# Kernel optimization log

Hardware: AMD Instinct MI355X
Metric: run time of the kernel (lower is better)

The kernel has to match this reference:

```python
import jax, jax.numpy as jnp
import numpy as np

# ---- constants mirroring ATSSPostProcessor defaults / metainfo ----
PRE_NMS_THRESH = 0.05
PRE_NMS_TOP_N = 1000
NMS_THRESH = 0.6
POST_TOP_N = 100
IMG_H, IMG_W = 800.0, 1216.0      # metainfo img_shape
BW_XY, BW_WH = 10.0, 5.0          # GLIP/ATSS box coder weights (10,10,5,5)
MAX_DWH = float(np.log(1000.0 / 16.0))
CLASS_OFFSET = 10000.0            # batched_nms class offset (> max coord)


def setup_inputs() -> dict:
    key = jax.random.key(0)
    k0, k1, k2, k3 = jax.random.split(key, 4)
    N, C, L, H, W = 8, 80, 256, 100, 152
    box_regression = jax.random.normal(k0, (N, 4, H, W), jnp.float32)
    centerness = jax.random.normal(k1, (N, 1, H, W), jnp.float32)
    box_cls = jax.random.normal(k2, (N, C, H, W), jnp.float32)
    dot_product_logits = jax.random.normal(k3, (N, H * W, L), jnp.float32)
    # stride-8 grid anchors with base size 64
    ys, xs = np.meshgrid(np.arange(H), np.arange(W), indexing='ij')
    cx, cy = (xs + 0.5) * 8.0, (ys + 0.5) * 8.0
    anchors = jnp.asarray(
        np.stack([cx - 32, cy - 32, cx + 32, cy + 32], -1).reshape(-1, 4),
        jnp.float32)
    # MEAN aggregation positive map: class j <- tokens [3j, 3j+1, 3j+2]
    pm = np.zeros((C, L), np.float32)
    for j in range(C):
        pm[j, 3 * j:3 * j + 3] = 1.0 / 3.0
    pos_map = jnp.asarray(pm)
    return dict(box_regression=box_regression, centerness=centerness,
                box_cls=box_cls, dot_product_logits=dot_product_logits,
                anchors=anchors, pos_map=pos_map)


def _decode(a, r):
    # delta_xywh decode with weights (10,10,5,5), clamped to img_shape
    aw, ah = a[..., 2] - a[..., 0], a[..., 3] - a[..., 1]
    acx, acy = a[..., 0] + 0.5 * aw, a[..., 1] + 0.5 * ah
    dx, dy = r[..., 0] / BW_XY, r[..., 1] / BW_XY
    dw = jnp.minimum(r[..., 2] / BW_WH, MAX_DWH)
    dh = jnp.minimum(r[..., 3] / BW_WH, MAX_DWH)
    pcx, pcy = dx * aw + acx, dy * ah + acy
    pw, ph = jnp.exp(dw) * aw, jnp.exp(dh) * ah
    x1 = jnp.clip(pcx - 0.5 * pw, 0.0, IMG_W)
    y1 = jnp.clip(pcy - 0.5 * ph, 0.0, IMG_H)
    x2 = jnp.clip(pcx + 0.5 * pw, 0.0, IMG_W)
    y2 = jnp.clip(pcy + 0.5 * ph, 0.0, IMG_H)
    return jnp.stack([x1, y1, x2, y2], -1)


def _iou_matrix(b):  # b: [K,4]
    area = (b[:, 2] - b[:, 0]) * (b[:, 3] - b[:, 1])
    ix1 = jnp.maximum(b[:, None, 0], b[None, :, 0])
    iy1 = jnp.maximum(b[:, None, 1], b[None, :, 1])
    ix2 = jnp.minimum(b[:, None, 2], b[None, :, 2])
    iy2 = jnp.minimum(b[:, None, 3], b[None, :, 3])
    inter = jnp.maximum(ix2 - ix1, 0.0) * jnp.maximum(iy2 - iy1, 0.0)
    return inter / (area[:, None] + area[None, :] - inter + 1e-6)


def _nms_single(boxes, scores, labels, valid):
    # class-aware greedy NMS (batched_nms) on fixed-size K candidates
    K = boxes.shape[0]
    s = jnp.where(valid, scores, -1.0)
    order = jnp.argsort(-s)
    b, s, l, v = boxes[order], s[order], labels[order], valid[order]
    ob = b + (l.astype(b.dtype) * CLASS_OFFSET)[:, None]
    iou = _iou_matrix(ob)
    ar = jnp.arange(K)

    def body(i, keep):
        sup = keep[i] & (iou[i] > NMS_THRESH) & (ar > i)
        return keep & ~sup

    keep = jax.lax.fori_loop(0, K, body, v)
    s2 = jnp.where(keep, s, -1.0)
    topv, topi = jax.lax.top_k(s2, POST_TOP_N)
    good = topv > 0.0
    fb = jnp.where(good[:, None], b[topi], 0.0)
    fs = jnp.where(good, topv, 0.0)
    fl = jnp.where(good, l[topi], 0)
    return fb, fs, fl


def reference(box_regression, centerness, box_cls, dot_product_logits,
              anchors, pos_map):
    N = box_regression.shape[0]
    C = pos_map.shape[0]
    HW = anchors.shape[0]
    # permute_and_flatten: [N,4,H,W] -> [N,HW,4]
    reg = box_regression.transpose(0, 2, 3, 1).reshape(N, HW, 4)
    ctr = jax.nn.sigmoid(centerness.reshape(N, HW))
    # sigmoid score fusion + MEAN grounding->od aggregation
    dp = jax.nn.sigmoid(dot_product_logits)            # [N,HW,L]
    scores = jnp.einsum('nkl,cl->nkc', dp, pos_map)    # [N,HW,C]
    cand = scores > PRE_NMS_THRESH
    fused = scores * ctr[:, :, None]
    # dynamic per-image topk over candidates == fixed-K masked top_k
    masked = jnp.where(cand, fused, -1.0).reshape(N, HW * C)
    vals, idx = jax.lax.top_k(masked, PRE_NMS_TOP_N)   # [N,K]
    valid = jnp.take_along_axis(cand.reshape(N, -1), idx, axis=1)
    loc = idx // C
    labels = idx % C + 1
    a = anchors[loc]                                           # [N,K,4]
    r = jnp.take_along_axis(reg, loc[..., None], axis=1)       # [N,K,4]
    boxes = _decode(a, r)
    sc = jnp.sqrt(jnp.maximum(vals, 0.0))
    w = boxes[..., 2] - boxes[..., 0]
    h = boxes[..., 3] - boxes[..., 1]
    valid = valid & (w > 0) & (h > 0)  # min_size = 0 filter
    # scale_factor = 1.0 -> boxes unchanged
    out_boxes, out_scores, out_labels = jax.vmap(_nms_single)(
        boxes, sc, labels, valid)
    return out_boxes, out_scores, out_labels
```

## Files before the change

kernel.cpp:

```cpp
#include <hip/hip_runtime.h>
#include <hip/hip_bf16.h>

#define NIMG 8
#define NC   80
#define NL   256
#define HWQ  15200
#define TOPK 1000
#define CAP  4096
#define SSORT 2048
#define NPOST 100
#define PERIMG (HWQ * NC)
#define TOTAL (NIMG * PERIMG)
#define SROW 32
#define SBLK32 (NIMG * HWQ / SROW)
#define PI4  (PERIMG / 4)
#define WPI  (PI4 / 64)
#define NWAVE (NIMG * WPI)
#define CBLK (TOTAL / 4 / 256)

__device__ __forceinline__ unsigned flipKey(float f) {
    unsigned u = __float_as_uint(f);
    return u ^ (((unsigned)((int)u >> 31)) | 0x80000000u);
}
__device__ __forceinline__ float unflipKey(unsigned k) {
    unsigned u = k ^ ((k & 0x80000000u) ? 0x80000000u : 0xFFFFFFFFu);
    return __uint_as_float(u);
}
__device__ __forceinline__ float sigmoidf(float x) {
    return 1.0f / (1.0f + expf(-x));
}

__global__ void __launch_bounds__(256)
kinit(const float* __restrict__ pm, unsigned* nnz, unsigned* tok, float* wt,
      unsigned* __restrict__ gh) {
    int g = blockIdx.x * 256 + threadIdx.x;
    if (g < NIMG * 4096) gh[g] = 0;
    if (g < NC) {
        int c = g;
        int cnt = 0;
        for (int l = 0; l < NL; ++l) {
            float v = pm[c * NL + l];
            if (v != 0.0f) { tok[cnt * NC + c] = l; wt[cnt * NC + c] = v; cnt++; }
        }
        nnz[c] = cnt;
    }
}

__global__ void __launch_bounds__(512)
kscoreh(const float* __restrict__ dp, const float* __restrict__ cent,
        const unsigned* __restrict__ nnz, const unsigned* __restrict__ tok,
        const float* __restrict__ wt, float* __restrict__ scores,
        unsigned* __restrict__ gh) {
    __shared__ unsigned h[4096];
    __shared__ float sctr[SROW];
    int t = threadIdx.x;
    for (int i = t; i < 4096; i += 512) h[i] = 0;
    long long base = (long long)blockIdx.x * SROW;
    if (t < SROW) sctr[t] = sigmoidf(cent[base + t]);
    long long obase = base * NC;
    const float* dpb = dp + base * NL;

    int  rr[5], cc[5], mm[5];
    int  tk[5][3];
    float wv[5][3], xv[5][3];
#pragma unroll
    for (int j = 0; j < 5; ++j) {
        int o = t + j * 512;
        rr[j] = o / NC; cc[j] = o - rr[j] * NC;
        mm[j] = (int)nnz[cc[j]];
        int c = cc[j];
        tk[j][0] = (int)tok[c] & 255;
        tk[j][1] = (int)tok[NC + c] & 255;
        tk[j][2] = (int)tok[2 * NC + c] & 255;
        wv[j][0] = wt[c]; wv[j][1] = wt[NC + c]; wv[j][2] = wt[2 * NC + c];
    }
#pragma unroll
    for (int j = 0; j < 5; ++j) {
        const float* row = dpb + rr[j] * NL;
        if (tk[j][1] == tk[j][0] + 1 && tk[j][2] == tk[j][0] + 2) {
            float3 v3 = *(const float3*)(row + tk[j][0]);
            xv[j][0] = v3.x; xv[j][1] = v3.y; xv[j][2] = v3.z;
        } else {
            xv[j][0] = row[tk[j][0]];
            xv[j][1] = row[tk[j][1]];
            xv[j][2] = row[tk[j][2]];
        }
    }
    __syncthreads();
#pragma unroll
    for (int j = 0; j < 5; ++j) {
        float acc = 0.0f;
        if (mm[j] == 3) {
            float s0 = sigmoidf(xv[j][0]);
            float s1 = sigmoidf(xv[j][1]);
            float s2 = sigmoidf(xv[j][2]);
            acc += s0 * wv[j][0]; acc += s1 * wv[j][1]; acc += s2 * wv[j][2];
        } else {
            const float* row = dpb + rr[j] * NL;
            for (int q = 0; q < mm[j]; ++q)
                acc += sigmoidf(row[tok[q * NC + cc[j]]]) * wt[q * NC + cc[j]];
        }
        float sc = (acc > 0.05f) ? acc * sctr[rr[j]] : -1.0f;
        scores[obase + t + j * 512] = sc;
        atomicAdd(&h[flipKey(sc) >> 20], 1u);
    }
    __syncthreads();
    int n = (int)(base / HWQ);
    for (int i = t; i < 4096; i += 512)
        if (h[i]) atomicAdd(&gh[n * 4096 + i], h[i]);
}

__global__ void kfind1(const unsigned* __restrict__ gh, unsigned* meta) {
    __shared__ unsigned h[4096];
    __shared__ unsigned psum[256];
    int n = blockIdx.x;
    for (int i = threadIdx.x; i < 4096; i += 256) h[i] = gh[n * 4096 + i];
    __syncthreads();
    unsigned s = 0;
    for (int i = 0; i < 16; ++i) s += h[threadIdx.x * 16 + i];
    psum[threadIdx.x] = s;
    __syncthreads();
    if (threadIdx.x == 0) {
        unsigned cum = 0, above = 0; int B = 0; bool done = false;
        for (int seg = 255; seg >= 0 && !done; --seg) {
            if (cum + psum[seg] >= TOPK) {
                for (int b = seg * 16 + 15; b >= seg * 16; --b) {
                    if (cum + h[b] >= TOPK) { B = b; above = cum; done = true; break; }
                    cum += h[b];
                }
            } else cum += psum[seg];
        }
        meta[n] = (unsigned)B;
        meta[8 + n] = above;
    }
}

__global__ void __launch_bounds__(256)
kcountM(const float4* __restrict__ scores4, const unsigned* __restrict__ meta,
        unsigned* __restrict__ wavecnt, unsigned long long* __restrict__ wavemask) {
    int i4 = blockIdx.x * 256 + threadIdx.x;
    int n = i4 / PI4;
    unsigned B = meta[n];
    float4 v = scores4[i4];
    bool s0 = (flipKey(v.x) >> 20) >= B;
    bool s1 = (flipKey(v.y) >> 20) >= B;
    bool s2 = (flipKey(v.z) >> 20) >= B;
    bool s3 = (flipKey(v.w) >> 20) >= B;
    unsigned long long m0 = __ballot(s0);
    unsigned long long m1 = __ballot(s1);
    unsigned long long m2 = __ballot(s2);
    unsigned long long m3 = __ballot(s3);
    if ((threadIdx.x & 63) == 0) {
        int w = i4 >> 6;
        wavemask[(size_t)w * 4 + 0] = m0;
        wavemask[(size_t)w * 4 + 1] = m1;
        wavemask[(size_t)w * 4 + 2] = m2;
        wavemask[(size_t)w * 4 + 3] = m3;
        wavecnt[w] = (unsigned)(__popcll(m0) + __popcll(m1)
                              + __popcll(m2) + __popcll(m3));
    }
}

__global__ void __launch_bounds__(1024)
kgather(const unsigned* __restrict__ wavecnt,
        const unsigned long long* __restrict__ wavemask,
        const float* __restrict__ scores, const unsigned* __restrict__ meta,
        unsigned long long* __restrict__ cand,
        unsigned long long* __restrict__ sorted) {
    __shared__ unsigned ps16[17];
    __shared__ unsigned long long sbuf[SSORT];
    __shared__ unsigned h[4096];
    __shared__ unsigned psum[256];
    __shared__ unsigned selcnt, Fbin;
    int n = blockIdx.x, t = threadIdx.x;
    int lane = t & 63, wid = t >> 6;
    const unsigned* wc = wavecnt + n * WPI;
    const unsigned long long* wm = wavemask + (size_t)n * WPI * 4;
    const float* sb = scores + (size_t)n * PERIMG;
    sbuf[t] = 0ULL; sbuf[t + 1024] = 0ULL;

    int s0 = t * 5;
    unsigned loc[5], vv[5]; unsigned sum = 0;
#pragma unroll
    for (int j = 0; j < 5; ++j) {
        int i = s0 + j;
        unsigned x = (i < WPI) ? wc[i] : 0u;
        vv[j] = x; loc[j] = sum; sum += x;
    }
    unsigned wincl = sum;
#pragma unroll
    for (int off = 1; off < 64; off <<= 1) {
        unsigned o = (unsigned)__shfl_up((int)wincl, off);
        if (lane >= off) wincl += o;
    }
    if (lane == 63) ps16[wid] = wincl;
    __syncthreads();
    if (t == 0) {
        unsigned c = 0;
        for (int w = 0; w < 16; ++w) { unsigned x = ps16[w]; ps16[w] = c; c += x; }
        ps16[16] = c;
    }
    __syncthreads();
    unsigned excl = ps16[wid] + (wincl - sum);
    unsigned total = ps16[16];
    int nsel;

    if (total <= SSORT) {
#pragma unroll
        for (int j = 0; j < 5; ++j) {
            int wl = s0 + j;
            if (wl < WPI && vv[j]) {
                unsigned off = excl + loc[j];
                const unsigned long long* mk = wm + (size_t)wl * 4;
#pragma unroll
                for (int e = 0; e < 4; ++e) {
                    unsigned long long m = mk[e];
                    while (m) {
                        int b = __ffsll(m) - 1; m &= m - 1;
                        int li = wl * 256 + b * 4 + e;
                        unsigned key = flipKey(sb[li]);
                        sbuf[off++] = ((unsigned long long)key << 32)
                                      | (unsigned)(~li);
                    }
                }
            }
        }
        nsel = (int)total;
        __syncthreads();
    } else {
        unsigned long long* cb = cand + (size_t)n * CAP;
#pragma unroll
        for (int j = 0; j < 5; ++j) {
            int wl = s0 + j;
            if (wl < WPI && vv[j]) {
                unsigned off = excl + loc[j];
                const unsigned long long* mk = wm + (size_t)wl * 4;
#pragma unroll
                for (int e = 0; e < 4; ++e) {
                    unsigned long long m = mk[e];
                    while (m) {
                        int b = __ffsll(m) - 1; m &= m - 1;
                        int li = wl * 256 + b * 4 + e;
                        unsigned key = flipKey(sb[li]);
                        if (off < CAP)
                            cb[off] = ((unsigned long long)key << 32)
                                      | (unsigned)(~li);
                        off++;
                    }
                }
            }
        }
        for (int i = t; i < 4096; i += 1024) h[i] = 0;
        if (t == 0) selcnt = 0;
        __syncthreads();
        int M = min((int)total, CAP);
        unsigned B = meta[n], above = meta[8 + n];
        for (int i = t; i < M; i += 1024) {
            unsigned key = (unsigned)(cb[i] >> 32);
            if ((key >> 20) == B) atomicAdd(&h[(key >> 8) & 0xFFFu], 1u);
        }
        __syncthreads();
        if (t < 256) {
            unsigned s = 0;
            for (int i = 0; i < 16; ++i) s += h[t * 16 + i];
            psum[t] = s;
        }
        __syncthreads();
        if (t == 0) {
            unsigned cum = above; int F = 0; bool done = false;
            for (int seg = 255; seg >= 0 && !done; --seg) {
                if (cum + psum[seg] >= TOPK) {
                    for (int b = seg * 16 + 15; b >= seg * 16; --b) {
                        if (cum + h[b] >= TOPK) { F = b; done = true; break; }
                        cum += h[b];
                    }
                } else cum += psum[seg];
            }
            Fbin = (unsigned)F;
        }
        __syncthreads();
        unsigned T24 = (meta[n] << 12) | Fbin;
        for (int i = t; i < M; i += 1024) {
            unsigned long long e = cb[i];
            unsigned key = (unsigned)(e >> 32);
            if ((key >> 8) >= T24) {
                unsigned p = atomicAdd(&selcnt, 1u);
                if (p < SSORT) sbuf[p] = e;
            }
        }
        __syncthreads();
        nsel = (int)selcnt;
    }

    int SN = (nsel <= 1024) ? 1024 : SSORT;
    for (int k = 2; k <= SN; k <<= 1) {
        for (int j = k >> 1; j > 0; j >>= 1) {
            for (int i = t; i < SN; i += 1024) {
                int l = i ^ j;
                if (l > i) {
                    unsigned long long a = sbuf[i], b = sbuf[l];
                    bool sw = ((i & k) == 0) ? (a < b) : (a > b);
                    if (sw) { sbuf[i] = b; sbuf[l] = a; }
                }
            }
            __syncthreads();
        }
    }
    if (t < TOPK) sorted[(n << 10) + t] = sbuf[t];
}

__global__ void __launch_bounds__(256)
kdecode(const unsigned long long* __restrict__ sorted,
        const float* __restrict__ anchors, const float* __restrict__ breg,
        float4* __restrict__ box4, float4* __restrict__ obx4,
        float* __restrict__ areag, unsigned* __restrict__ lblkeep) {
    int gid = blockIdx.x * 256 + threadIdx.x;
    if (gid >= NIMG * TOPK) return;
    int n = gid / TOPK, r = gid - n * TOPK;
    int o = (n << 10) + r;
    unsigned long long e = sorted[o];
    unsigned key = (unsigned)(e >> 32);
    bool real = key > 0x80000000u;
    unsigned li = ~(unsigned)(e & 0xFFFFFFFFu);
    unsigned k = li / NC, c = li - k * NC;
    int label = (int)c + 1;
    float x1 = 0, y1 = 0, x2 = 0, y2 = 0;
    bool val = false;
    if (real) {
        float a0 = anchors[k * 4 + 0], a1 = anchors[k * 4 + 1];
        float a2 = anchors[k * 4 + 2], a3 = anchors[k * 4 + 3];
        float r0 = breg[(n * 4 + 0) * HWQ + k];
        float r1 = breg[(n * 4 + 1) * HWQ + k];
        float r2 = breg[(n * 4 + 2) * HWQ + k];
        float r3 = breg[(n * 4 + 3) * HWQ + k];
        float aw = a2 - a0, ah = a3 - a1;
        float acx = a0 + 0.5f * aw, acy = a1 + 0.5f * ah;
        float dx = r0 / 10.0f, dy = r1 / 10.0f;
        float dw = fminf(r2 / 5.0f, 4.135166556742356f);
        float dh = fminf(r3 / 5.0f, 4.135166556742356f);
        float pcx = dx * aw + acx, pcy = dy * ah + acy;
        float pw = expf(dw) * aw, ph = expf(dh) * ah;
        x1 = fminf(fmaxf(pcx - 0.5f * pw, 0.0f), 1216.0f);
        y1 = fminf(fmaxf(pcy - 0.5f * ph, 0.0f), 800.0f);
        x2 = fminf(fmaxf(pcx + 0.5f * pw, 0.0f), 1216.0f);
        y2 = fminf(fmaxf(pcy + 0.5f * ph, 0.0f), 800.0f);
        val = (x2 - x1 > 0.0f) && (y2 - y1 > 0.0f);
    }
    box4[o] = make_float4(x1, y1, x2, y2);
    float off = (float)label * 10000.0f;
    float o0 = x1 + off, o1 = y1 + off, o2 = x2 + off, o3 = y2 + off;
    obx4[o] = make_float4(o0, o1, o2, o3);
    areag[o] = (o2 - o0) * (o3 - o1);
    lblkeep[o] = (unsigned)(real ? label : 0) | ((val ? 1u : 0u) << 16);
}

__global__ void __launch_bounds__(1024)
knms2(const unsigned long long* __restrict__ sorted,
      const float4* __restrict__ obx4, const float* __restrict__ areag,
      const unsigned* __restrict__ lblkeep, const float4* __restrict__ box4,
      float* __restrict__ outBoxes, float* __restrict__ outScores,
      float* __restrict__ outLabels) {
    __shared__ float ob0[TOPK], ob1[TOPK], ob2[TOPK], ob3[TOPK], area[TOPK];
    __shared__ unsigned long long sup[TOPK];
    __shared__ unsigned long long cbits[NC * 16];
    __shared__ unsigned short lbl[TOPK];
    __shared__ unsigned char  keepf[TOPK];
    __shared__ unsigned short wrank[TOPK];
    __shared__ unsigned short clist[TOPK];
    __shared__ unsigned short cstart[NC + 1];
    __shared__ unsigned ccnt[NC];
    __shared__ int ps16[17];
    __shared__ int smax;

    int n = blockIdx.x, t = threadIdx.x;
    int lane = t & 63, wid = t >> 6;
    for (int i = t; i < NC * 16; i += 1024) cbits[i] = 0ULL;
    if (t == 0) smax = 0;
    if (t < TOPK) {
        int o = (n << 10) + t;
        float4 ob = obx4[o];
        ob0[t] = ob.x; ob1[t] = ob.y; ob2[t] = ob.z; ob3[t] = ob.w;
        area[t] = areag[o];
        unsigned lk = lblkeep[o];
        lbl[t] = (unsigned short)(lk & 0xFFFFu);
        keepf[t] = (unsigned char)(lk >> 16);
        sup[t] = 0ULL;
    }
    __syncthreads();

    if (t < TOPK && lbl[t])
        atomicOr(&cbits[(lbl[t] - 1) * 16 + (t >> 6)], 1ull << (t & 63));
    __syncthreads();
    if (t < NC) {
        unsigned s = 0;
#pragma unroll
        for (int w = 0; w < 16; ++w) s += (unsigned)__popcll(cbits[t * 16 + w]);
        ccnt[t] = s;
    }
    __syncthreads();
    if (t < NC) atomicMax(&smax, (int)ccnt[t]);
    __syncthreads();
    if (t == 0) {
        unsigned s = 0;
        for (int c = 0; c < NC; ++c) { cstart[c] = (unsigned short)s; s += ccnt[c]; }
        cstart[NC] = (unsigned short)s;
    }
    __syncthreads();
    if (t < TOPK && lbl[t]) {
        int my = lbl[t] - 1;
        int w = 0;
        int hi = t >> 6;
        for (int q = 0; q < hi; ++q) w += (int)__popcll(cbits[my * 16 + q]);
        w += (int)__popcll(cbits[my * 16 + hi] & ((1ull << (t & 63)) - 1ull));
        wrank[t] = (unsigned short)w;
        clist[cstart[my] + w] = (unsigned short)t;
    }
    __syncthreads();

    if (smax <= 64) {
        if (t < TOPK && lbl[t]) {
            int base = cstart[lbl[t] - 1];
            int w = wrank[t];
            float A0 = ob0[t], A1 = ob1[t], A2 = ob2[t], A3 = ob3[t], Aa = area[t];
            unsigned long long m = 0ULL;
            for (int j = 0; j < w; ++j) {
                int ib = clist[base + j];
                float iw = fminf(A2, ob2[ib]) - fmaxf(A0, ob0[ib]);
                float ih = fminf(A3, ob3[ib]) - fmaxf(A1, ob1[ib]);
                float inter = fmaxf(iw, 0.0f) * fmaxf(ih, 0.0f);
                float denom = Aa + area[ib] - inter + 1e-6f;
                if (inter / denom > 0.6f) m |= (1ull << j);
            }
            sup[t] = m;
        }
        __syncthreads();
        if (t < NC) {
            unsigned long long kb = 0ULL;
            int base = cstart[t], mc = (int)ccnt[t];
            for (int w = 0; w < mc; ++w) {
                int i = clist[base + w];
                bool kp = keepf[i] && ((sup[i] & kb) == 0ULL);
                keepf[i] = kp ? 1 : 0;
                if (kp) kb |= (1ull << w);
            }
        }
    } else {
        __syncthreads();
        if (t < NC) {
            int s0 = cstart[t], s1 = s0 + (int)ccnt[t];
            for (int a = s0; a < s1; ++a) {
                int ia = clist[a];
                if (!keepf[ia]) continue;
                float A0 = ob0[ia], A1 = ob1[ia], A2 = ob2[ia], A3 = ob3[ia];
                float Aa = area[ia];
                for (int b = a + 1; b < s1; ++b) {
                    int ib = clist[b];
                    if (!keepf[ib]) continue;
                    float iw = fminf(A2, ob2[ib]) - fmaxf(A0, ob0[ib]);
                    float ih = fminf(A3, ob3[ib]) - fmaxf(A1, ob1[ib]);
                    float inter = fmaxf(iw, 0.0f) * fmaxf(ih, 0.0f);
                    float denom = Aa + area[ib] - inter + 1e-6f;
                    if (inter / denom > 0.6f) keepf[ib] = 0;
                }
            }
        }
    }
    __syncthreads();

    int v = (t < TOPK) ? (int)keepf[t] : 0;
    int incl = v;
#pragma unroll
    for (int off = 1; off < 64; off <<= 1) {
        int o = __shfl_up(incl, off);
        if (lane >= off) incl += o;
    }
    if (lane == 63) ps16[wid] = incl;
    __syncthreads();
    if (t == 0) {
        int c = 0;
        for (int w = 0; w < 16; ++w) { int x = ps16[w]; ps16[w] = c; c += x; }
        ps16[16] = c;
    }
    __syncthreads();
    int myincl = incl + ps16[wid];
    int total = ps16[16];

    if (t < TOPK && keepf[t]) {
        int q = myincl - 1;
        if (q < NPOST) {
            int o = (n << 10) + t;
            float4 b = box4[o];
            float fused = unflipKey((unsigned)(sorted[o] >> 32));
            outBoxes[(n * NPOST + q) * 4 + 0] = b.x;
            outBoxes[(n * NPOST + q) * 4 + 1] = b.y;
            outBoxes[(n * NPOST + q) * 4 + 2] = b.z;
            outBoxes[(n * NPOST + q) * 4 + 3] = b.w;
            outScores[n * NPOST + q] = sqrtf(fmaxf(fused, 0.0f));
            outLabels[n * NPOST + q] = (float)lbl[t];
        }
    }
    if (t < NPOST && t >= total) {
        outBoxes[(n * NPOST + t) * 4 + 0] = 0.0f;
        outBoxes[(n * NPOST + t) * 4 + 1] = 0.0f;
        outBoxes[(n * NPOST + t) * 4 + 2] = 0.0f;
        outBoxes[(n * NPOST + t) * 4 + 3] = 0.0f;
        outScores[n * NPOST + t] = 0.0f;
        outLabels[n * NPOST + t] = 0.0f;
    }
}

extern "C" void kernel_launch(void* const* d_in, const int* in_sizes, int n_in,
                              void* d_out, int out_size, void* d_ws, size_t ws_size,
                              hipStream_t stream) {
    const float* breg = (const float*)d_in[0];
    const float* cent = (const float*)d_in[1];
    const float* dp   = (const float*)d_in[3];
    const float* anc  = (const float*)d_in[4];
    const float* pm   = (const float*)d_in[5];

    char* ws = (char*)d_ws;
    size_t off_scores   = 0;
    size_t off_gh       = off_scores + (size_t)TOTAL * 4;
    size_t off_meta     = off_gh + (size_t)NIMG * 4096 * 4;
    size_t off_cand     = off_meta + 128;
    size_t off_nnz      = off_cand + (size_t)NIMG * CAP * 8;
    size_t off_tok      = off_nnz + 512;
    size_t off_wt       = off_tok + (size_t)NC * NL * 4;
    size_t off_wavecnt  = off_wt + (size_t)NC * NL * 4;
    size_t off_wavemask = off_wavecnt + (size_t)NWAVE * 4 + 64;
    size_t needed       = off_wavemask + (size_t)NWAVE * 32;
    if (ws_size < needed) return;

    size_t off_sorted = off_scores;
    size_t off_box4   = off_sorted + (size_t)NIMG * 1024 * 8;
    size_t off_obx4   = off_box4 + (size_t)NIMG * 1024 * 16;
    size_t off_area   = off_obx4 + (size_t)NIMG * 1024 * 16;
    size_t off_lblk   = off_area + (size_t)NIMG * 1024 * 4;

    float*    scores  = (float*)(ws + off_scores);
    unsigned* gh      = (unsigned*)(ws + off_gh);
    unsigned* meta    = (unsigned*)(ws + off_meta);
    unsigned long long* cand = (unsigned long long*)(ws + off_cand);
    unsigned* nnz     = (unsigned*)(ws + off_nnz);
    unsigned* tok     = (unsigned*)(ws + off_tok);
    float*    wt      = (float*)(ws + off_wt);
    unsigned* wavecnt = (unsigned*)(ws + off_wavecnt);
    unsigned long long* wavemask = (unsigned long long*)(ws + off_wavemask);
    unsigned long long* sorted = (unsigned long long*)(ws + off_sorted);
    float4*   box4    = (float4*)(ws + off_box4);
    float4*   obx4    = (float4*)(ws + off_obx4);
    float*    areag   = (float*)(ws + off_area);
    unsigned* lblkeep = (unsigned*)(ws + off_lblk);

    kinit<<<128, 256, 0, stream>>>(pm, nnz, tok, wt, gh);
    kscoreh<<<SBLK32, 512, 0, stream>>>(dp, cent, nnz, tok, wt, scores, gh);
    kfind1<<<NIMG, 256, 0, stream>>>(gh, meta);
    kcountM<<<CBLK, 256, 0, stream>>>((const float4*)scores, meta,
                                      wavecnt, wavemask);
    kgather<<<NIMG, 1024, 0, stream>>>(wavecnt, wavemask, scores, meta,
                                       cand, sorted);
    kdecode<<<(NIMG * TOPK + 255) / 256, 256, 0, stream>>>(sorted, anc, breg,
                                                           box4, obx4, areag, lblkeep);

    float* outBoxes  = (float*)d_out;
    float* outScores = outBoxes + NIMG * NPOST * 4;
    float* outLabels = outScores + NIMG * NPOST;
    knms2<<<NIMG, 1024, 0, stream>>>(sorted, obx4, areag, lblkeep, box4,
                                     outBoxes, outScores, outLabels);
}
```

Baseline: 185.4 us.

## Record per-chunk score maxima to skip below-threshold chunks in count pass

The scoring kernel now computes a wave-level maximum sort key for each 256-element chunk and writes it to a new workspace buffer. The count kernel checks this maximum against the image's top-k bucket threshold and exits early for chunks that cannot hold a candidate, writing a zero count and skipping the score read and ballots. Separately, histogram atomics for sub-threshold (-1) scores are merged into one ballot-based add per wave, to ease LDS contention on that bucket. In exchange, the scoring kernel pays for a per-wave shuffle reduction, an LDS atomicMax and a small extra global write.

```diff
diff --git a/kernel.cpp b/kernel.cpp
--- a/kernel.cpp
+++ b/kernel.cpp
@@ -17,6 +17,7 @@
 #define WPI  (PI4 / 64)
 #define NWAVE (NIMG * WPI)
 #define CBLK (TOTAL / 4 / 256)
+#define NEGBKT 0x407u
 
 __device__ __forceinline__ unsigned flipKey(float f) {
     unsigned u = __float_as_uint(f);
@@ -50,11 +51,14 @@
 kscoreh(const float* __restrict__ dp, const float* __restrict__ cent,
         const unsigned* __restrict__ nnz, const unsigned* __restrict__ tok,
         const float* __restrict__ wt, float* __restrict__ scores,
-        unsigned* __restrict__ gh) {
+        unsigned* __restrict__ gh, unsigned* __restrict__ chunkmax) {
     __shared__ unsigned h[4096];
     __shared__ float sctr[SROW];
+    __shared__ unsigned cmaxs[10];
     int t = threadIdx.x;
+    int lane = t & 63, wid = t >> 6;
     for (int i = t; i < 4096; i += 512) h[i] = 0;
+    if (t < 10) cmaxs[t] = 0;
     long long base = (long long)blockIdx.x * SROW;
     if (t < SROW) sctr[t] = sigmoidf(cent[base + t]);
     long long obase = base * NC;
@@ -102,12 +106,26 @@
         }
         float sc = (acc > 0.05f) ? acc * sctr[rr[j]] : -1.0f;
         scores[obase + t + j * 512] = sc;
-        atomicAdd(&h[flipKey(sc) >> 20], 1u);
+        unsigned key = flipKey(sc);
+        bool isneg = (sc == -1.0f);
+        unsigned long long nb = __ballot(isneg);
+        if (isneg) {
+            if (lane == __ffsll(nb) - 1)
+                atomicAdd(&h[NEGBKT], (unsigned)__popcll(nb));
+        } else {
+            atomicAdd(&h[key >> 20], 1u);
+        }
+        unsigned wmax = key;
+#pragma unroll
+        for (int off = 1; off < 64; off <<= 1)
+            wmax = max(wmax, (unsigned)__shfl_xor((int)wmax, off));
+        if (lane == 0) atomicMax(&cmaxs[2 * j + (wid >> 2)], wmax);
     }
     __syncthreads();
     int n = (int)(base / HWQ);
     for (int i = t; i < 4096; i += 512)
         if (h[i]) atomicAdd(&gh[n * 4096 + i], h[i]);
+    if (t < 10) chunkmax[blockIdx.x * 10 + t] = cmaxs[t];
 }
 
 __global__ void kfind1(const unsigned* __restrict__ gh, unsigned* meta) {
@@ -137,10 +155,18 @@
 
 __global__ void __launch_bounds__(256)
 kcountM(const float4* __restrict__ scores4, const unsigned* __restrict__ meta,
+        const unsigned* __restrict__ chunkmax,
         unsigned* __restrict__ wavecnt, unsigned long long* __restrict__ wavemask) {
     int i4 = blockIdx.x * 256 + threadIdx.x;
     int n = i4 / PI4;
+    int w = i4 >> 6;
+    int lane = threadIdx.x & 63;
     unsigned B = meta[n];
+    unsigned cm = chunkmax[w];
+    if ((cm >> 20) < B) {
+        if (lane == 0) wavecnt[w] = 0;
+        return;
+    }
     float4 v = scores4[i4];
     bool s0 = (flipKey(v.x) >> 20) >= B;
     bool s1 = (flipKey(v.y) >> 20) >= B;
@@ -150,8 +176,7 @@
     unsigned long long m1 = __ballot(s1);
     unsigned long long m2 = __ballot(s2);
     unsigned long long m3 = __ballot(s3);
-    if ((threadIdx.x & 63) == 0) {
-        int w = i4 >> 6;
+    if (lane == 0) {
         wavemask[(size_t)w * 4 + 0] = m0;
         wavemask[(size_t)w * 4 + 1] = m1;
         wavemask[(size_t)w * 4 + 2] = m2;
@@ -528,7 +553,8 @@
     size_t off_wt       = off_tok + (size_t)NC * NL * 4;
     size_t off_wavecnt  = off_wt + (size_t)NC * NL * 4;
     size_t off_wavemask = off_wavecnt + (size_t)NWAVE * 4 + 64;
-    size_t needed       = off_wavemask + (size_t)NWAVE * 32;
+    size_t off_cmax     = off_wavemask + (size_t)NWAVE * 32;
+    size_t needed       = off_cmax + (size_t)NWAVE * 4 + 64;
     if (ws_size < needed) return;
 
     size_t off_sorted = off_scores;
@@ -546,6 +572,7 @@
     float*    wt      = (float*)(ws + off_wt);
     unsigned* wavecnt = (unsigned*)(ws + off_wavecnt);
     unsigned long long* wavemask = (unsigned long long*)(ws + off_wavemask);
+    unsigned* cmax    = (unsigned*)(ws + off_cmax);
     unsigned long long* sorted = (unsigned long long*)(ws + off_sorted);
     float4*   box4    = (float4*)(ws + off_box4);
     float4*   obx4    = (float4*)(ws + off_obx4);
@@ -553,9 +580,10 @@
     unsigned* lblkeep = (unsigned*)(ws + off_lblk);
 
     kinit<<<128, 256, 0, stream>>>(pm, nnz, tok, wt, gh);
-    kscoreh<<<SBLK32, 512, 0, stream>>>(dp, cent, nnz, tok, wt, scores, gh);
+    kscoreh<<<SBLK32, 512, 0, stream>>>(dp, cent, nnz, tok, wt, scores,
+                                        gh, cmax);
     kfind1<<<NIMG, 256, 0, stream>>>(gh, meta);
-    kcountM<<<CBLK, 256, 0, stream>>>((const float4*)scores, meta,
+    kcountM<<<CBLK, 256, 0, stream>>>((const float4*)scores, meta, cmax,
                                       wavecnt, wavemask);
     kgather<<<NIMG, 1024, 0, stream>>>(wavecnt, wavemask, scores, meta,
                                        cand, sorted);
```

After: 189.5 us. 1.02x slower.
